# Optimization experiments

Hardware: AMD Instinct MI355X
Metric: run time of the kernel (lower is better)

## Reference

```python
import jax, jax.numpy as jnp
import numpy as np

D_MODEL, D_STATE, D_CONV, EXPAND = 1024, 64, 4, 2
D_INNER = D_MODEL * EXPAND
BATCH, SEQ = 4, 4096


def setup_inputs() -> dict:
    key = jax.random.key(0)
    ks = jax.random.split(key, 9)
    s = lambda fan_in: 1.0 / np.sqrt(fan_in)
    return {
        "x": jax.random.normal(ks[0], (BATCH, SEQ, D_MODEL), jnp.float32),
        "in_proj_w": jax.random.uniform(ks[1], (D_MODEL, 2 * D_INNER), jnp.float32, -s(D_MODEL), s(D_MODEL)),
        "conv_w": jax.random.uniform(ks[2], (D_INNER, 1, D_CONV), jnp.float32, -s(D_CONV), s(D_CONV)),
        "conv_b": jax.random.uniform(ks[3], (D_INNER,), jnp.float32, -s(D_CONV), s(D_CONV)),
        "sB_w": jax.random.uniform(ks[4], (D_INNER, D_STATE), jnp.float32, -s(D_INNER), s(D_INNER)),
        "sC_w": jax.random.uniform(ks[5], (D_INNER, D_STATE), jnp.float32, -s(D_INNER), s(D_INNER)),
        "sdelta_w": jax.random.uniform(ks[6], (D_INNER, D_INNER), jnp.float32, -s(D_INNER), s(D_INNER)),
        "sdelta_b": jax.random.uniform(ks[7], (D_INNER,), jnp.float32, -s(D_INNER), s(D_INNER)),
        "A_log": jnp.log(jnp.arange(1, D_STATE + 1, dtype=jnp.float32)),
        "D_param": jnp.ones((D_INNER,), jnp.float32),
        "out_proj_w": jax.random.uniform(ks[8], (D_INNER, D_MODEL), jnp.float32, -s(D_INNER), s(D_INNER)),
        "out_proj_b": jnp.zeros((D_MODEL,), jnp.float32),
    }


def reference(x, in_proj_w, conv_w, conv_b, sB_w, sC_w, sdelta_w, sdelta_b, A_log, D_param, out_proj_w, out_proj_b):
    batch, seq_len, _ = x.shape
    d_inner = conv_w.shape[0]
    k = conv_w.shape[-1]
    # input projection + gate split
    x_proj = x @ in_proj_w                         # (B, L, 2*Di)
    x_ssm, x_gate = jnp.split(x_proj, 2, axis=-1)
    # causal depthwise conv1d: torch pads (k-1) both sides then truncates to L == left-pad only
    xc = jnp.transpose(x_ssm, (0, 2, 1))           # (B, Di, L)
    xc = jax.lax.conv_general_dilated(
        xc, conv_w, window_strides=(1,), padding=[(k - 1, 0)],
        dimension_numbers=("NCH", "OIH", "NCH"), feature_group_count=d_inner)
    xc = xc + conv_b[None, :, None]
    xc = jax.nn.silu(jnp.transpose(xc, (0, 2, 1)))  # (B, L, Di)
    # selection mechanism
    A = -jnp.exp(A_log)                            # (N,)
    Bm = xc @ sB_w                                 # (B, L, N)
    Cm = xc @ sC_w                                 # (B, L, N)
    delta = jax.nn.softplus(xc @ sdelta_w + sdelta_b)  # (B, L, Di)
    # selective scan over time with lax.scan
    def step(h, inp):
        xt, dt, Bt, Ct = inp                       # (B,Di),(B,Di),(B,N),(B,N)
        Abar = jnp.exp(dt[..., None] * A)          # (B, Di, N)
        h = Abar * h + (dt * xt)[..., None] * Bt[:, None, :]
        y = jnp.einsum("bdn,bn->bd", h, Ct)
        return h, y
    h0 = jnp.zeros((batch, d_inner, A.shape[0]), x.dtype)
    xs = (jnp.swapaxes(xc, 0, 1), jnp.swapaxes(delta, 0, 1),
          jnp.swapaxes(Bm, 0, 1), jnp.swapaxes(Cm, 0, 1))
    _, ys = jax.lax.scan(step, h0, xs)             # (L, B, Di)
    y = jnp.swapaxes(ys, 0, 1) + xc * D_param      # skip via D
    y = y * jax.nn.silu(x_gate)                    # gating
    return y @ out_proj_w + out_proj_b             # (B, L, d_model)
```

## Files before the change

kernel.cpp:

```cpp
#include <hip/hip_runtime.h>
#include <math.h>


typedef __bf16 bf16;
typedef __attribute__((__ext_vector_type__(8))) __bf16 bf16x8;
typedef __attribute__((__ext_vector_type__(4))) __bf16 bf16x4;
typedef __attribute__((__ext_vector_type__(4))) float  f32x4;

#define DM     1024
#define DI     2048
#define NPROJ  4096
#define LSEQ   4096
#define NB     4
#define NS     64
#define NCH    32
#define TC     128

__device__ __forceinline__ void gl_lds16(const bf16* g, bf16* l) {
  __builtin_amdgcn_global_load_lds(
      (const __attribute__((address_space(1))) void*)g,
      (__attribute__((address_space(3))) void*)l, 16, 0, 0);
}

__global__ __launch_bounds__(256) void cast_bf16(const float* __restrict__ in,
                                                 bf16* __restrict__ out) {
  size_t i = ((size_t)blockIdx.x * 256 + threadIdx.x) * 4;
  float4 v = *(const float4*)&in[i];
  bf16x4 t = {(bf16)v.x, (bf16)v.y, (bf16)v.z, (bf16)v.w};
  *(bf16x4*)&out[i] = t;
}

__global__ __launch_bounds__(256) void transpose_w(const float* __restrict__ in,
                                                   bf16* __restrict__ out,
                                                   int R, int C) {
  __shared__ float tile[32][33];
  int bc = blockIdx.x * 32, br = blockIdx.y * 32;
  int tx = threadIdx.x & 31, ty = threadIdx.x >> 5;
#pragma unroll
  for (int i = 0; i < 32; i += 8)
    tile[ty + i][tx] = in[(size_t)(br + ty + i) * C + bc + tx];
  __syncthreads();
#pragma unroll
  for (int i = 0; i < 32; i += 8)
    out[(size_t)(bc + ty + i) * R + br + tx] = (bf16)tile[tx][ty + i];
}

__global__ __launch_bounds__(256) void conv_w_tr(const float* __restrict__ w,
                                                 float* __restrict__ wt) {
  int d = blockIdx.x * 256 + threadIdx.x;
  float4 v = *(const float4*)&w[d * 4];
  wt[0 * DI + d] = v.x;
  wt[1 * DI + d] = v.y;
  wt[2 * DI + d] = v.z;
  wt[3 * DI + d] = v.w;
}

template <int EPI>
__global__ __launch_bounds__(256) void gemm_bt(const bf16* __restrict__ A,
                                               const bf16* __restrict__ Wt,
                                               const float* __restrict__ bias,
                                               void* __restrict__ Cp,
                                               void* __restrict__ Cp2,
                                               int M, int N, int Nsplit, int K) {
  __shared__ __align__(16) bf16 As[128 * 64];
  __shared__ __align__(16) bf16 Bs[128 * 64];
  const int tid = threadIdx.x;
  const int m0 = blockIdx.x * 128, n0 = blockIdx.y * 128;
  const int wave = tid >> 6, lane = tid & 63;
  const int wm = (wave & 1) * 64, wn = (wave >> 1) * 64;
  const int lr = lane & 15, lq = lane >> 4;
  const int sw = lr & 7;

  f32x4 acc[4][4];
  const f32x4 z4 = {0.f, 0.f, 0.f, 0.f};
#pragma unroll
  for (int i = 0; i < 4; i++)
#pragma unroll
    for (int j = 0; j < 4; j++) acc[i][j] = z4;

  for (int k0 = 0; k0 < K; k0 += 64) {
#pragma unroll
    for (int it = 0; it < 4; it++) {
      int ci = wave * 4 + it;
      int c = ci * 64 + lane;
      int row = c >> 3;
      int col8 = ((c & 7) ^ (row & 7)) * 8;
      gl_lds16(&A[(size_t)(m0 + row) * K + k0 + col8], &As[ci * 512]);
      gl_lds16(&Wt[(size_t)(n0 + row) * K + k0 + col8], &Bs[ci * 512]);
    }
    __syncthreads();
#pragma unroll
    for (int kk = 0; kk < 64; kk += 32) {
      bf16x8 af[4], bfr[4];
#pragma unroll
      for (int i = 0; i < 4; i++)
        af[i] = *(const bf16x8*)
            &As[(wm + i * 16 + lr) * 64 + ((((kk >> 3) + lq) ^ sw) * 8)];
#pragma unroll
      for (int j = 0; j < 4; j++)
        bfr[j] = *(const bf16x8*)
            &Bs[(wn + j * 16 + lr) * 64 + ((((kk >> 3) + lq) ^ sw) * 8)];
#pragma unroll
      for (int i = 0; i < 4; i++)
#pragma unroll
        for (int j = 0; j < 4; j++)
          acc[i][j] = __builtin_amdgcn_mfma_f32_16x16x32_bf16(af[i], bfr[j],
                                                              acc[i][j], 0, 0, 0);
    }
    __syncthreads();
  }

#pragma unroll
  for (int i = 0; i < 4; i++) {
#pragma unroll
    for (int j = 0; j < 4; j++) {
#pragma unroll
      for (int r = 0; r < 4; r++) {
        int row = m0 + wm + i * 16 + lq * 4 + r;
        int col = n0 + wn + j * 16 + lr;
        float v = acc[i][j][r];
        if (EPI == 0) {
          if (col < Nsplit)
            ((bf16*)Cp)[(size_t)row * Nsplit + col] = (bf16)v;
          else
            ((bf16*)Cp2)[(size_t)row * (N - Nsplit) + (col - Nsplit)] = (bf16)v;
        } else if (EPI == 2) {
          if (col < Nsplit) {
            v += bias[col];
            v = (v > 20.f) ? v : log1pf(__expf(v));
            ((bf16*)Cp)[(size_t)row * Nsplit + col] = (bf16)v;
          } else {
            ((float*)Cp2)[(size_t)row * (N - Nsplit) + (col - Nsplit)] = v;
          }
        } else {
          v += bias[col];
          ((float*)Cp)[(size_t)row * N + col] = v;
        }
      }
    }
  }
}

__global__ __launch_bounds__(256) void conv_silu(const bf16* __restrict__ xssm,
                                                 const float* __restrict__ wt,
                                                 const float* __restrict__ cb,
                                                 bf16* __restrict__ xc) {
  size_t idx = (size_t)blockIdx.x * 256 + threadIdx.x;
  int d0 = (int)(idx & (DI / 8 - 1)) * 8;
  size_t bt = idx >> 8;
  int t = (int)(bt & (LSEQ - 1));
  const bf16* base = xssm + bt * DI + d0;
  bf16x8 xm3 = {}, xm2 = {}, xm1 = {};
  if (t >= 3) xm3 = *(const bf16x8*)&base[-3 * DI];
  if (t >= 2) xm2 = *(const bf16x8*)&base[-2 * DI];
  if (t >= 1) xm1 = *(const bf16x8*)&base[-1 * DI];
  bf16x8 x0 = *(const bf16x8*)&base[0];
  float w0[8], w1[8], w2[8], w3[8], cbv[8];
  *(float4*)&w0[0] = *(const float4*)&wt[0 * DI + d0];
  *(float4*)&w0[4] = *(const float4*)&wt[0 * DI + d0 + 4];
  *(float4*)&w1[0] = *(const float4*)&wt[1 * DI + d0];
  *(float4*)&w1[4] = *(const float4*)&wt[1 * DI + d0 + 4];
  *(float4*)&w2[0] = *(const float4*)&wt[2 * DI + d0];
  *(float4*)&w2[4] = *(const float4*)&wt[2 * DI + d0 + 4];
  *(float4*)&w3[0] = *(const float4*)&wt[3 * DI + d0];
  *(float4*)&w3[4] = *(const float4*)&wt[3 * DI + d0 + 4];
  *(float4*)&cbv[0] = *(const float4*)&cb[d0];
  *(float4*)&cbv[4] = *(const float4*)&cb[d0 + 4];
  bf16x8 o;
#pragma unroll
  for (int j = 0; j < 8; j++) {
    float acc = cbv[j];
    acc = fmaf((float)xm3[j], w0[j], acc);
    acc = fmaf((float)xm2[j], w1[j], acc);
    acc = fmaf((float)xm1[j], w2[j], acc);
    acc = fmaf((float)x0[j], w3[j], acc);
    acc = acc / (1.f + __expf(-acc));
    o[j] = (bf16)acc;
  }
  *(bf16x8*)&xc[bt * DI + d0] = o;
}


__global__ __launch_bounds__(256) void scan_pass1(const bf16* __restrict__ delta,
                                                  const bf16* __restrict__ xc,
                                                  const float* __restrict__ BC,
                                                  float* __restrict__ S,
                                                  float* __restrict__ SD) {
  __shared__ __align__(16) float Bsh[32][64];
  __shared__ __align__(16) bf16 Dsh[32][128];
  __shared__ __align__(16) bf16 Xsh[32][128];
  const int b = blockIdx.z, c = blockIdx.y;
  const int tid = threadIdx.x;
  const int lane = tid & 63, wv = tid >> 6;
  const int half = lane >> 5, dn = lane & 31;
  const int dl = wv * 32 + dn;
  const int d0 = blockIdx.x * 128;
  const int d = d0 + dl;
  float h[32];
#pragma unroll
  for (int j = 0; j < 32; j++) h[j] = 0.f;
  float sumdt = 0.f;

  for (int qt = 0; qt < 4; qt++) {
    const int tbase = c * TC + qt * 32;
    __syncthreads();
#pragma unroll
    for (int it = 0; it < 2; it++) {
      int e = tid + it * 256;
      int tt = e >> 4, n4 = (e & 15) * 4;
      *(float4*)&Bsh[tt][n4] =
          *(const float4*)&BC[((size_t)b * LSEQ + tbase + tt) * 128 + n4];
    }
#pragma unroll
    for (int it = 0; it < 2; it++) {
      int e = tid + it * 256;
      int tt = e >> 4, c8 = (e & 15) * 8;
      size_t ro = ((size_t)b * LSEQ + tbase + tt) * DI + d0;
      *(bf16x8*)&Dsh[tt][c8] = *(const bf16x8*)&delta[ro + c8];
      *(bf16x8*)&Xsh[tt][c8] = *(const bf16x8*)&xc[ro + c8];
    }
    __syncthreads();
    for (int tt = 0; tt < 32; tt++) {
      float dt = (float)Dsh[tt][dl];
      float xv = (float)Xsh[tt][dl];
      float dx = dt * xv;
      float r = __expf(-dt);
      sumdt += dt;
      float r2 = r * r, r4 = r2 * r2;
      float r8 = r4 * r4, r16 = r8 * r8, r32 = r16 * r16;
      float base = half ? (r32 * r) : r;
      float p0 = base, p1 = base * r, p2 = base * r2, p3 = p1 * r2;
#pragma unroll
      for (int g = 0; g < 8; g++) {
        float4 Bv = *(const float4*)&Bsh[tt][half * 32 + g * 4];
        h[4 * g + 0] = fmaf(p0, h[4 * g + 0], dx * Bv.x);
        h[4 * g + 1] = fmaf(p1, h[4 * g + 1], dx * Bv.y);
        h[4 * g + 2] = fmaf(p2, h[4 * g + 2], dx * Bv.z);
        h[4 * g + 3] = fmaf(p3, h[4 * g + 3], dx * Bv.w);
        if (g != 7) { p0 *= r4; p1 *= r4; p2 *= r4; p3 *= r4; }
      }
    }
  }
  size_t sb = (((size_t)b * NCH + c) * NS + half * 32) * DI + d;
#pragma unroll
  for (int j = 0; j < 32; j++) S[sb + (size_t)j * DI] = h[j];
  if (half == 0) SD[((size_t)b * NCH + c) * DI + d] = sumdt;
}

__global__ __launch_bounds__(256) void scan_pass2(float* __restrict__ S,
                                                  const float* __restrict__ SD) {
  const int d = blockIdx.x * 256 + threadIdx.x;
  const int n = blockIdx.y, b = blockIdx.z;
  const float nf = -(float)(n + 1);
  float h = 0.f;
  for (int c = 0; c < NCH; c++) {
    size_t o = (((size_t)b * NCH + c) * NS + n) * DI + d;
    float s = S[o];
    S[o] = h;
    float sd = SD[((size_t)b * NCH + c) * DI + d];
    h = __expf(nf * sd) * h + s;
  }
}

__global__ __launch_bounds__(256) void scan_pass3(const bf16* __restrict__ delta,
                                                  const bf16* __restrict__ xc,
                                                  const float* __restrict__ BC,
                                                  const float* __restrict__ Hin,
                                                  const bf16* __restrict__ xgate,
                                                  const float* __restrict__ Dp,
                                                  bf16* __restrict__ yg) {
  __shared__ __align__(16) float Bsh[32][64];
  __shared__ __align__(16) float Csh[32][64];
  __shared__ __align__(16) bf16 Dsh[32][128];
  __shared__ __align__(16) bf16 Xsh[32][128];
  __shared__ __align__(16) bf16 Gsh[32][128];
  const int b = blockIdx.z, c = blockIdx.y;
  const int tid = threadIdx.x;
  const int lane = tid & 63, wv = tid >> 6;
  const int half = lane >> 5, dn = lane & 31;
  const int dl = wv * 32 + dn;
  const int d0 = blockIdx.x * 128;
  const int d = d0 + dl;
  float h[32];
  size_t hb = (((size_t)b * NCH + c) * NS + half * 32) * DI + d;
#pragma unroll
  for (int j = 0; j < 32; j++) h[j] = Hin[hb + (size_t)j * DI];
  const float Dv = Dp[d];

  for (int qt = 0; qt < 4; qt++) {
    const int tbase = c * TC + qt * 32;
    __syncthreads();
#pragma unroll
    for (int it = 0; it < 2; it++) {
      int e = tid + it * 256;
      int tt = e >> 4, n4 = (e & 15) * 4;
      size_t rowo = ((size_t)b * LSEQ + tbase + tt) * 128;
      *(float4*)&Bsh[tt][n4] = *(const float4*)&BC[rowo + n4];
      *(float4*)&Csh[tt][n4] = *(const float4*)&BC[rowo + 64 + n4];
    }
#pragma unroll
    for (int it = 0; it < 2; it++) {
      int e = tid + it * 256;
      int tt = e >> 4, c8 = (e & 15) * 8;
      size_t ro = ((size_t)b * LSEQ + tbase + tt) * DI + d0;
      *(bf16x8*)&Dsh[tt][c8] = *(const bf16x8*)&delta[ro + c8];
      *(bf16x8*)&Xsh[tt][c8] = *(const bf16x8*)&xc[ro + c8];
      *(bf16x8*)&Gsh[tt][c8] = *(const bf16x8*)&xgate[ro + c8];
    }
    __syncthreads();
    for (int tt = 0; tt < 32; tt++) {
      size_t o = ((size_t)b * LSEQ + tbase + tt) * DI + d;
      float dt = (float)Dsh[tt][dl];
      float xv = (float)Xsh[tt][dl];
      float dx = dt * xv;
      float r = __expf(-dt);
      float r2 = r * r, r4 = r2 * r2;
      float r8 = r4 * r4, r16 = r8 * r8, r32 = r16 * r16;
      float base = half ? (r32 * r) : r;
      float p0 = base, p1 = base * r, p2 = base * r2, p3 = p1 * r2;
      float y0 = 0.f, y1 = 0.f, y2 = 0.f, y3 = 0.f;
#pragma unroll
      for (int g = 0; g < 8; g++) {
        float4 Bv = *(const float4*)&Bsh[tt][half * 32 + g * 4];
        float4 Cv = *(const float4*)&Csh[tt][half * 32 + g * 4];
        h[4 * g + 0] = fmaf(p0, h[4 * g + 0], dx * Bv.x); y0 = fmaf(h[4 * g + 0], Cv.x, y0);
        h[4 * g + 1] = fmaf(p1, h[4 * g + 1], dx * Bv.y); y1 = fmaf(h[4 * g + 1], Cv.y, y1);
        h[4 * g + 2] = fmaf(p2, h[4 * g + 2], dx * Bv.z); y2 = fmaf(h[4 * g + 2], Cv.z, y2);
        h[4 * g + 3] = fmaf(p3, h[4 * g + 3], dx * Bv.w); y3 = fmaf(h[4 * g + 3], Cv.w, y3);
        if (g != 7) { p0 *= r4; p1 *= r4; p2 *= r4; p3 *= r4; }
      }
      float y = (y0 + y1) + (y2 + y3);
      y += __shfl_xor(y, 32, 64);
      if (half == 0) {
        y += xv * Dv;
        float g = (float)Gsh[tt][dl];
        y *= g / (1.f + __expf(-g));
        yg[o] = (bf16)y;
      }
    }
  }
}

extern "C" void kernel_launch(void* const* d_in, const int* in_sizes, int n_in,
                              void* d_out, int out_size, void* d_ws, size_t ws_size,
                              hipStream_t stream) {
  const float* x         = (const float*)d_in[0];
  const float* in_proj_w = (const float*)d_in[1];
  const float* conv_w    = (const float*)d_in[2];
  const float* conv_b    = (const float*)d_in[3];
  const float* sB_w      = (const float*)d_in[4];
  const float* sC_w      = (const float*)d_in[5];
  const float* sdelta_w  = (const float*)d_in[6];
  const float* sdelta_b  = (const float*)d_in[7];
  const float* D_param    = (const float*)d_in[9];
  const float* out_proj_w = (const float*)d_in[10];
  const float* out_proj_b = (const float*)d_in[11];
  float* out = (float*)d_out;

  char* ws = (char*)d_ws;
  size_t off = 0;
  auto alloc = [&](size_t bytes) {
    char* p = ws + off;
    off += (bytes + 255) & ~(size_t)255;
    return p;
  };
  bf16*  W1t     = (bf16*)alloc((size_t)NPROJ * DM * 2);
  bf16*  WdBC    = (bf16*)alloc((size_t)(DI + 128) * DI * 2);
  bf16*  Wot     = (bf16*)alloc((size_t)DM * DI * 2);
  bf16*  xb      = (bf16*)alloc((size_t)NB * LSEQ * DM * 2);
  float* conv_wt = (float*)alloc((size_t)4 * DI * 4);
  bf16*  WBCt    = WdBC + (size_t)DI * DI;
  const size_t fixed_bytes = off;

  const size_t PB = (size_t)LSEQ * DI * 2
                  + (size_t)LSEQ * DI * 2
                  + (size_t)LSEQ * DI * 2
                  + (size_t)LSEQ * DI * 2
                  + (size_t)LSEQ * 128 * 4
                  + (size_t)NCH * NS * DI * 4
                  + (size_t)NCH * DI * 4
                  + 8 * 256;
  int G = (ws_size >= fixed_bytes + 4 * PB) ? 4
        : (ws_size >= fixed_bytes + 2 * PB) ? 2 : 1;

  bf16*  xssm  = (bf16*)alloc((size_t)G * LSEQ * DI * 2);
  bf16*  xgate = (bf16*)alloc((size_t)G * LSEQ * DI * 2);
  bf16*  xc    = (bf16*)alloc((size_t)G * LSEQ * DI * 2);
  bf16*  delta = (bf16*)alloc((size_t)G * LSEQ * DI * 2);
  float* BC    = (float*)alloc((size_t)G * LSEQ * 128 * 4);
  float* S     = (float*)alloc((size_t)G * NCH * NS * DI * 4);
  float* SD    = (float*)alloc((size_t)G * NCH * DI * 4);
  bf16*  yg    = xssm;

  cast_bf16<<<(NB * (size_t)LSEQ * DM) / 1024, 256, 0, stream>>>(x, xb);
  transpose_w<<<dim3(NPROJ / 32, DM / 32), 256, 0, stream>>>(in_proj_w, W1t, DM, NPROJ);
  transpose_w<<<dim3(DI / 32, DI / 32), 256, 0, stream>>>(sdelta_w, WdBC, DI, DI);
  transpose_w<<<dim3(NS / 32, DI / 32), 256, 0, stream>>>(sB_w, WBCt, DI, NS);
  transpose_w<<<dim3(NS / 32, DI / 32), 256, 0, stream>>>(sC_w, WBCt + (size_t)NS * DI, DI, NS);
  transpose_w<<<dim3(DM / 32, DI / 32), 256, 0, stream>>>(out_proj_w, Wot, DI, DM);
  conv_w_tr<<<DI / 256, 256, 0, stream>>>(conv_w, conv_wt);

  const int M = G * LSEQ;
  for (int g = 0; g < NB / G; g++) {
    const bf16* xg_in = xb + (size_t)g * G * LSEQ * DM;
    float* out_g = out + (size_t)g * G * LSEQ * DM;

    gemm_bt<0><<<dim3(M / 128, NPROJ / 128), 256, 0, stream>>>(
        xg_in, W1t, nullptr, xssm, xgate, M, NPROJ, DI, DM);
    conv_silu<<<((size_t)M * DI / 8) / 256, 256, 0, stream>>>(xssm, conv_wt,
                                                              conv_b, xc);
    gemm_bt<2><<<dim3(M / 128, (DI + 128) / 128), 256, 0, stream>>>(
        xc, WdBC, sdelta_b, delta, BC, M, DI + 128, DI, DI);
    scan_pass1<<<dim3(DI / 128, NCH, G), 256, 0, stream>>>(delta, xc, BC, S, SD);
    scan_pass2<<<dim3(DI / 256, NS, G), 256, 0, stream>>>(S, SD);
    scan_pass3<<<dim3(DI / 128, NCH, G), 256, 0, stream>>>(delta, xc, BC, S, xgate,
                                                           D_param, yg);
    gemm_bt<3><<<dim3(M / 128, DM / 128), 256, 0, stream>>>(
        yg, Wot, out_proj_b, out_g, nullptr, M, DM, DM, DI);
  }
}
```

Baseline: 1.445 ms.

## Give each scan thread all 64 states and swizzle GEMM block order

```diff
diff --git a/kernel.cpp b/kernel.cpp
--- a/kernel.cpp
+++ b/kernel.cpp
@@ -65,7 +65,11 @@
   __shared__ __align__(16) bf16 As[128 * 64];
   __shared__ __align__(16) bf16 Bs[128 * 64];
   const int tid = threadIdx.x;
-  const int m0 = blockIdx.x * 128, n0 = blockIdx.y * 128;
+  const int bid = (int)blockIdx.x;
+  const int cpx = (int)gridDim.x >> 3;
+  const int swz = (bid & 7) * cpx + (bid >> 3);
+  const int nMB = M >> 7;
+  const int m0 = (swz % nMB) * 128, n0 = (swz / nMB) * 128;
   const int wave = tid >> 6, lane = tid & 63;
   const int wm = (wave & 1) * 64, wn = (wave >> 1) * 64;
   const int lr = lane & 15, lq = lane >> 4;
@@ -187,18 +191,12 @@
                                                   float* __restrict__ S,
                                                   float* __restrict__ SD) {
   __shared__ __align__(16) float Bsh[32][64];
-  __shared__ __align__(16) bf16 Dsh[32][128];
-  __shared__ __align__(16) bf16 Xsh[32][128];
   const int b = blockIdx.z, c = blockIdx.y;
   const int tid = threadIdx.x;
-  const int lane = tid & 63, wv = tid >> 6;
-  const int half = lane >> 5, dn = lane & 31;
-  const int dl = wv * 32 + dn;
-  const int d0 = blockIdx.x * 128;
-  const int d = d0 + dl;
-  float h[32];
-#pragma unroll
-  for (int j = 0; j < 32; j++) h[j] = 0.f;
+  const int d = blockIdx.x * 256 + tid;
+  float h[64];
+#pragma unroll
+  for (int j = 0; j < 64; j++) h[j] = 0.f;
   float sumdt = 0.f;
 
   for (int qt = 0; qt < 4; qt++) {
@@ -211,40 +209,31 @@
       *(float4*)&Bsh[tt][n4] =
           *(const float4*)&BC[((size_t)b * LSEQ + tbase + tt) * 128 + n4];
     }
-#pragma unroll
-    for (int it = 0; it < 2; it++) {
-      int e = tid + it * 256;
-      int tt = e >> 4, c8 = (e & 15) * 8;
-      size_t ro = ((size_t)b * LSEQ + tbase + tt) * DI + d0;
-      *(bf16x8*)&Dsh[tt][c8] = *(const bf16x8*)&delta[ro + c8];
-      *(bf16x8*)&Xsh[tt][c8] = *(const bf16x8*)&xc[ro + c8];
-    }
-    __syncthreads();
-    for (int tt = 0; tt < 32; tt++) {
-      float dt = (float)Dsh[tt][dl];
-      float xv = (float)Xsh[tt][dl];
+    __syncthreads();
+    size_t o = ((size_t)b * LSEQ + tbase) * DI + d;
+    for (int tt = 0; tt < 32; tt++, o += DI) {
+      float dt = (float)delta[o];
+      float xv = (float)xc[o];
       float dx = dt * xv;
       float r = __expf(-dt);
       sumdt += dt;
       float r2 = r * r, r4 = r2 * r2;
-      float r8 = r4 * r4, r16 = r8 * r8, r32 = r16 * r16;
-      float base = half ? (r32 * r) : r;
-      float p0 = base, p1 = base * r, p2 = base * r2, p3 = p1 * r2;
-#pragma unroll
-      for (int g = 0; g < 8; g++) {
-        float4 Bv = *(const float4*)&Bsh[tt][half * 32 + g * 4];
+      float p0 = r, p1 = r2, p2 = r2 * r, p3 = r4;
+#pragma unroll
+      for (int g = 0; g < 16; g++) {
+        float4 Bv = *(const float4*)&Bsh[tt][g * 4];
         h[4 * g + 0] = fmaf(p0, h[4 * g + 0], dx * Bv.x);
         h[4 * g + 1] = fmaf(p1, h[4 * g + 1], dx * Bv.y);
         h[4 * g + 2] = fmaf(p2, h[4 * g + 2], dx * Bv.z);
         h[4 * g + 3] = fmaf(p3, h[4 * g + 3], dx * Bv.w);
-        if (g != 7) { p0 *= r4; p1 *= r4; p2 *= r4; p3 *= r4; }
+        if (g != 15) { p0 *= r4; p1 *= r4; p2 *= r4; p3 *= r4; }
       }
     }
   }
-  size_t sb = (((size_t)b * NCH + c) * NS + half * 32) * DI + d;
-#pragma unroll
-  for (int j = 0; j < 32; j++) S[sb + (size_t)j * DI] = h[j];
-  if (half == 0) SD[((size_t)b * NCH + c) * DI + d] = sumdt;
+  size_t sb = (((size_t)b * NCH + c) * NS) * DI + d;
+#pragma unroll
+  for (int j = 0; j < 64; j++) S[sb + (size_t)j * DI] = h[j];
+  SD[((size_t)b * NCH + c) * DI + d] = sumdt;
 }
 
 __global__ __launch_bounds__(256) void scan_pass2(float* __restrict__ S,
@@ -271,20 +260,13 @@
                                                   bf16* __restrict__ yg) {
   __shared__ __align__(16) float Bsh[32][64];
   __shared__ __align__(16) float Csh[32][64];
-  __shared__ __align__(16) bf16 Dsh[32][128];
-  __shared__ __align__(16) bf16 Xsh[32][128];
-  __shared__ __align__(16) bf16 Gsh[32][128];
   const int b = blockIdx.z, c = blockIdx.y;
   const int tid = threadIdx.x;
-  const int lane = tid & 63, wv = tid >> 6;
-  const int half = lane >> 5, dn = lane & 31;
-  const int dl = wv * 32 + dn;
-  const int d0 = blockIdx.x * 128;
-  const int d = d0 + dl;
-  float h[32];
-  size_t hb = (((size_t)b * NCH + c) * NS + half * 32) * DI + d;
-#pragma unroll
-  for (int j = 0; j < 32; j++) h[j] = Hin[hb + (size_t)j * DI];
+  const int d = blockIdx.x * 256 + tid;
+  float h[64];
+  size_t hb = (((size_t)b * NCH + c) * NS) * DI + d;
+#pragma unroll
+  for (int j = 0; j < 64; j++) h[j] = Hin[hb + (size_t)j * DI];
   const float Dv = Dp[d];
 
   for (int qt = 0; qt < 4; qt++) {
@@ -298,45 +280,31 @@
       *(float4*)&Bsh[tt][n4] = *(const float4*)&BC[rowo + n4];
       *(float4*)&Csh[tt][n4] = *(const float4*)&BC[rowo + 64 + n4];
     }
-#pragma unroll
-    for (int it = 0; it < 2; it++) {
-      int e = tid + it * 256;
-      int tt = e >> 4, c8 = (e & 15) * 8;
-      size_t ro = ((size_t)b * LSEQ + tbase + tt) * DI + d0;
-      *(bf16x8*)&Dsh[tt][c8] = *(const bf16x8*)&delta[ro + c8];
-      *(bf16x8*)&Xsh[tt][c8] = *(const bf16x8*)&xc[ro + c8];
-      *(bf16x8*)&Gsh[tt][c8] = *(const bf16x8*)&xgate[ro + c8];
-    }
-    __syncthreads();
-    for (int tt = 0; tt < 32; tt++) {
-      size_t o = ((size_t)b * LSEQ + tbase + tt) * DI + d;
-      float dt = (float)Dsh[tt][dl];
-      float xv = (float)Xsh[tt][dl];
+    __syncthreads();
+    size_t o = ((size_t)b * LSEQ + tbase) * DI + d;
+    for (int tt = 0; tt < 32; tt++, o += DI) {
+      float dt = (float)delta[o];
+      float xv = (float)xc[o];
       float dx = dt * xv;
       float r = __expf(-dt);
       float r2 = r * r, r4 = r2 * r2;
-      float r8 = r4 * r4, r16 = r8 * r8, r32 = r16 * r16;
-      float base = half ? (r32 * r) : r;
-      float p0 = base, p1 = base * r, p2 = base * r2, p3 = p1 * r2;
+      float p0 = r, p1 = r2, p2 = r2 * r, p3 = r4;
       float y0 = 0.f, y1 = 0.f, y2 = 0.f, y3 = 0.f;
 #pragma unroll
-      for (int g = 0; g < 8; g++) {
-        float4 Bv = *(const float4*)&Bsh[tt][half * 32 + g * 4];
-        float4 Cv = *(const float4*)&Csh[tt][half * 32 + g * 4];
+      for (int g = 0; g < 16; g++) {
+        float4 Bv = *(const float4*)&Bsh[tt][g * 4];
+        float4 Cv = *(const float4*)&Csh[tt][g * 4];
         h[4 * g + 0] = fmaf(p0, h[4 * g + 0], dx * Bv.x); y0 = fmaf(h[4 * g + 0], Cv.x, y0);
         h[4 * g + 1] = fmaf(p1, h[4 * g + 1], dx * Bv.y); y1 = fmaf(h[4 * g + 1], Cv.y, y1);
         h[4 * g + 2] = fmaf(p2, h[4 * g + 2], dx * Bv.z); y2 = fmaf(h[4 * g + 2], Cv.z, y2);
         h[4 * g + 3] = fmaf(p3, h[4 * g + 3], dx * Bv.w); y3 = fmaf(h[4 * g + 3], Cv.w, y3);
-        if (g != 7) { p0 *= r4; p1 *= r4; p2 *= r4; p3 *= r4; }
+        if (g != 15) { p0 *= r4; p1 *= r4; p2 *= r4; p3 *= r4; }
       }
       float y = (y0 + y1) + (y2 + y3);
-      y += __shfl_xor(y, 32, 64);
-      if (half == 0) {
-        y += xv * Dv;
-        float g = (float)Gsh[tt][dl];
-        y *= g / (1.f + __expf(-g));
-        yg[o] = (bf16)y;
-      }
+      y += xv * Dv;
+      float gv = (float)xgate[o];
+      y *= gv / (1.f + __expf(-gv));
+      yg[o] = (bf16)y;
     }
   }
 }
@@ -405,17 +373,17 @@
     const bf16* xg_in = xb + (size_t)g * G * LSEQ * DM;
     float* out_g = out + (size_t)g * G * LSEQ * DM;
 
-    gemm_bt<0><<<dim3(M / 128, NPROJ / 128), 256, 0, stream>>>(
+    gemm_bt<0><<<(M / 128) * (NPROJ / 128), 256, 0, stream>>>(
         xg_in, W1t, nullptr, xssm, xgate, M, NPROJ, DI, DM);
     conv_silu<<<((size_t)M * DI / 8) / 256, 256, 0, stream>>>(xssm, conv_wt,
                                                               conv_b, xc);
-    gemm_bt<2><<<dim3(M / 128, (DI + 128) / 128), 256, 0, stream>>>(
+    gemm_bt<2><<<(M / 128) * ((DI + 128) / 128), 256, 0, stream>>>(
         xc, WdBC, sdelta_b, delta, BC, M, DI + 128, DI, DI);
-    scan_pass1<<<dim3(DI / 128, NCH, G), 256, 0, stream>>>(delta, xc, BC, S, SD);
+    scan_pass1<<<dim3(DI / 256, NCH, G), 256, 0, stream>>>(delta, xc, BC, S, SD);
     scan_pass2<<<dim3(DI / 256, NS, G), 256, 0, stream>>>(S, SD);
-    scan_pass3<<<dim3(DI / 128, NCH, G), 256, 0, stream>>>(delta, xc, BC, S, xgate,
+    scan_pass3<<<dim3(DI / 256, NCH, G), 256, 0, stream>>>(delta, xc, BC, S, xgate,
                                                            D_param, yg);
-    gemm_bt<3><<<dim3(M / 128, DM / 128), 256, 0, stream>>>(
+    gemm_bt<3><<<(M / 128) * (DM / 128), 256, 0, stream>>>(
         yg, Wot, out_proj_b, out_g, nullptr, M, DM, DM, DI);
   }
 }
```

Measured after the change: 1.564 ms. +8.2%, slower.

## Add 256x256-tile pipelined bf16 GEMM for delta/B/C projection

Applied to the files above, without the earlier changes.

```diff
diff --git a/kernel.cpp b/kernel.cpp
--- a/kernel.cpp
+++ b/kernel.cpp
@@ -15,6 +15,7 @@
 #define NS     64
 #define NCH    32
 #define TC     128
+#define NPAD   2304
 
 __device__ __forceinline__ void gl_lds16(const bf16* g, bf16* l) {
   __builtin_amdgcn_global_load_lds(
@@ -124,17 +125,134 @@
             ((bf16*)Cp)[(size_t)row * Nsplit + col] = (bf16)v;
           else
             ((bf16*)Cp2)[(size_t)row * (N - Nsplit) + (col - Nsplit)] = (bf16)v;
-        } else if (EPI == 2) {
-          if (col < Nsplit) {
-            v += bias[col];
-            v = (v > 20.f) ? v : log1pf(__expf(v));
-            ((bf16*)Cp)[(size_t)row * Nsplit + col] = (bf16)v;
-          } else {
-            ((float*)Cp2)[(size_t)row * (N - Nsplit) + (col - Nsplit)] = v;
-          }
         } else {
           v += bias[col];
           ((float*)Cp)[(size_t)row * N + col] = v;
+        }
+      }
+    }
+  }
+}
+
+__global__ __launch_bounds__(512, 2) void gemm256(const bf16* __restrict__ A,
+                                                  const bf16* __restrict__ Wt,
+                                                  const float* __restrict__ bias,
+                                                  void* __restrict__ Cp,
+                                                  void* __restrict__ Cp2,
+                                                  int M, int Nsplit, int Nreal,
+                                                  int K) {
+  __shared__ __align__(16) bf16 As[2][2][128 * 64];
+  __shared__ __align__(16) bf16 Bs[2][2][128 * 64];
+  const int tid = threadIdx.x;
+  const int wave = tid >> 6, lane = tid & 63;
+  const int m0 = blockIdx.x * 256, n0 = blockIdx.y * 256;
+  const int wm = (wave >> 2) << 7;
+  const int wn = (wave & 3) << 6;
+  const int rhA = wave >> 2;
+  const int rhB = wn >> 7;
+  const int rbB = wn & 64;
+  const int lr = lane & 15, lq = lane >> 4;
+  const int sw = lr & 7;
+  const int NT = K >> 6;
+
+  f32x4 acc[8][4];
+  const f32x4 z4 = {0.f, 0.f, 0.f, 0.f};
+#pragma unroll
+  for (int i = 0; i < 8; ++i)
+#pragma unroll
+    for (int j = 0; j < 4; ++j) acc[i][j] = z4;
+
+  auto stage = [&](const bf16* G, bf16* lds, int gr0, int kt) {
+#pragma unroll
+    for (int it = 0; it < 2; ++it) {
+      const int sb = it * 512 + wave * 64;
+      const int s = sb + lane;
+      const int row = s >> 3, pos = s & 7;
+      gl_lds16(&G[(size_t)(gr0 + row) * K + kt * 64 + ((pos ^ (row & 7)) * 8)],
+               lds + sb * 8);
+    }
+  };
+
+  bf16x8 af[4], bfr[4];
+  auto readA = [&](int cur, int kk, int mh) {
+#pragma unroll
+    for (int i = 0; i < 4; ++i)
+      af[i] = *(const bf16x8*)
+          &As[cur][rhA][(mh * 64 + i * 16 + lr) * 64 +
+                        ((((kk >> 3) + lq) ^ sw) * 8)];
+  };
+  auto readB = [&](int cur, int kk) {
+#pragma unroll
+    for (int j = 0; j < 4; ++j)
+      bfr[j] = *(const bf16x8*)
+          &Bs[cur][rhB][(rbB + j * 16 + lr) * 64 +
+                        ((((kk >> 3) + lq) ^ sw) * 8)];
+  };
+  auto mma = [&](int mh) {
+#pragma unroll
+    for (int i = 0; i < 4; ++i)
+#pragma unroll
+      for (int j = 0; j < 4; ++j)
+        acc[mh * 4 + i][j] = __builtin_amdgcn_mfma_f32_16x16x32_bf16(
+            af[i], bfr[j], acc[mh * 4 + i][j], 0, 0, 0);
+  };
+
+  stage(Wt, &Bs[0][0][0], n0, 0);
+  stage(Wt, &Bs[0][1][0], n0 + 128, 0);
+  stage(A, &As[0][0][0], m0, 0);
+  stage(A, &As[0][1][0], m0 + 128, 0);
+  stage(Wt, &Bs[1][0][0], n0, 1);
+  asm volatile("s_waitcnt vmcnt(2)" ::: "memory");
+  __builtin_amdgcn_s_barrier();
+
+  for (int t = 0; t < NT; ++t) {
+    const int cur = t & 1, nxt = cur ^ 1;
+    readB(cur, 0); readA(cur, 0, 0);
+    if (t + 1 < NT) stage(Wt, &Bs[nxt][1][0], n0 + 128, t + 1);
+    __builtin_amdgcn_s_barrier();
+    asm volatile("s_waitcnt lgkmcnt(0)" ::: "memory");
+    __builtin_amdgcn_s_setprio(1); mma(0); __builtin_amdgcn_s_setprio(0);
+    __builtin_amdgcn_s_barrier();
+    readA(cur, 0, 1);
+    if (t + 1 < NT) stage(A, &As[nxt][0][0], m0, t + 1);
+    __builtin_amdgcn_s_barrier();
+    asm volatile("s_waitcnt lgkmcnt(0)" ::: "memory");
+    __builtin_amdgcn_s_setprio(1); mma(1); __builtin_amdgcn_s_setprio(0);
+    __builtin_amdgcn_s_barrier();
+    readB(cur, 32); readA(cur, 32, 0);
+    if (t + 1 < NT) stage(A, &As[nxt][1][0], m0 + 128, t + 1);
+    __builtin_amdgcn_s_barrier();
+    asm volatile("s_waitcnt lgkmcnt(0)" ::: "memory");
+    __builtin_amdgcn_s_setprio(1); mma(0); __builtin_amdgcn_s_setprio(0);
+    __builtin_amdgcn_s_barrier();
+    readA(cur, 32, 1);
+    if (t + 2 < NT) stage(Wt, &Bs[cur][0][0], n0, t + 2);
+    __builtin_amdgcn_s_barrier();
+    asm volatile("s_waitcnt lgkmcnt(0)" ::: "memory");
+    __builtin_amdgcn_s_setprio(1); mma(1); __builtin_amdgcn_s_setprio(0);
+    if (t + 2 < NT) {
+      asm volatile("s_waitcnt vmcnt(2)" ::: "memory");
+    } else if (t + 1 < NT) {
+      asm volatile("s_waitcnt vmcnt(0)" ::: "memory");
+    }
+    __builtin_amdgcn_s_barrier();
+  }
+
+#pragma unroll
+  for (int mi = 0; mi < 8; ++mi) {
+#pragma unroll
+    for (int j = 0; j < 4; ++j) {
+#pragma unroll
+      for (int r = 0; r < 4; ++r) {
+        const int row = m0 + wm + mi * 16 + lq * 4 + r;
+        const int col = n0 + wn + j * 16 + lr;
+        float v = acc[mi][j][r];
+        if (col < Nsplit) {
+          v += bias[col];
+          v = (v > 20.f) ? v : log1pf(__expf(v));
+          ((bf16*)Cp)[(size_t)row * Nsplit + col] = (bf16)v;
+        } else if (col < Nreal) {
+          ((float*)Cp2)[(size_t)row * (Nreal - Nsplit) + (col - Nsplit)] = v;
         }
       }
     }
@@ -365,7 +483,7 @@
     return p;
   };
   bf16*  W1t     = (bf16*)alloc((size_t)NPROJ * DM * 2);
-  bf16*  WdBC    = (bf16*)alloc((size_t)(DI + 128) * DI * 2);
+  bf16*  WdBC    = (bf16*)alloc((size_t)NPAD * DI * 2);
   bf16*  Wot     = (bf16*)alloc((size_t)DM * DI * 2);
   bf16*  xb      = (bf16*)alloc((size_t)NB * LSEQ * DM * 2);
   float* conv_wt = (float*)alloc((size_t)4 * DI * 4);
@@ -409,8 +527,8 @@
         xg_in, W1t, nullptr, xssm, xgate, M, NPROJ, DI, DM);
     conv_silu<<<((size_t)M * DI / 8) / 256, 256, 0, stream>>>(xssm, conv_wt,
                                                               conv_b, xc);
-    gemm_bt<2><<<dim3(M / 128, (DI + 128) / 128), 256, 0, stream>>>(
-        xc, WdBC, sdelta_b, delta, BC, M, DI + 128, DI, DI);
+    gemm256<<<dim3(M / 256, NPAD / 256), 512, 0, stream>>>(
+        xc, WdBC, sdelta_b, delta, BC, M, DI, DI + 128, DI);
     scan_pass1<<<dim3(DI / 128, NCH, G), 256, 0, stream>>>(delta, xc, BC, S, SD);
     scan_pass2<<<dim3(DI / 256, NS, G), 256, 0, stream>>>(S, SD);
     scan_pass3<<<dim3(DI / 128, NCH, G), 256, 0, stream>>>(delta, xc, BC, S, xgate,
```

Result: faster. 1.337 ms (-7.5%).
